# Performance work log

Measured on AMD Instinct MI355X. Metric: run time of the kernel, lower is better.

The kernel has to match this reference:

```python
import jax, jax.numpy as jnp
import numpy as np

NEG_SLOPE = 0.2  # PyG GATConv default leaky_relu slope


def _gat_conv(x, src, dst, W, a_src, a_dst, b, num_nodes, heads, out_dim):
    # x: [N, F_in] -> h: [N, H, C]
    h = (x @ W).reshape(num_nodes, heads, out_dim)
    alpha_src = jnp.sum(h * a_src, axis=-1)  # [N, H]
    alpha_dst = jnp.sum(h * a_dst, axis=-1)  # [N, H]
    # per-edge unnormalized attention logits [E, H]
    alpha = jax.nn.leaky_relu(alpha_src[src] + alpha_dst[dst], NEG_SLOPE)
    # segment softmax over incoming edges of each destination node
    amax = jax.ops.segment_max(alpha, dst, num_segments=num_nodes)  # [N, H]
    e = jnp.exp(alpha - amax[dst])
    denom = jax.ops.segment_sum(e, dst, num_segments=num_nodes)  # [N, H]
    attn = e / denom[dst]  # every node has a self-loop, denom > 0
    # scatter-aggregate messages [E, H, C] -> [N, H, C]
    msg = h[src] * attn[:, :, None]
    out = jax.ops.segment_sum(msg, dst, num_segments=num_nodes)
    return out.reshape(num_nodes, heads * out_dim) + b


def setup_inputs() -> dict:
    key = jax.random.key(0)
    ks = jax.random.split(key, 12)
    N, F_in, H, C1, C2 = 100000, 128, 4, 32, 16
    E = 1600000
    x = jax.random.normal(ks[0], (N, F_in), dtype=jnp.float32)
    edge_index = jax.random.randint(ks[1], (2, E), 0, N, dtype=jnp.int64)
    s1 = 1.0 / np.sqrt(F_in)
    s2 = 1.0 / np.sqrt(H * C1)
    W1 = jax.random.normal(ks[2], (F_in, H * C1), dtype=jnp.float32) * s1
    a_src1 = jax.random.normal(ks[3], (H, C1), dtype=jnp.float32) * s1
    a_dst1 = jax.random.normal(ks[4], (H, C1), dtype=jnp.float32) * s1
    b1 = jnp.zeros((H * C1,), dtype=jnp.float32)
    W2 = jax.random.normal(ks[5], (H * C1, C2), dtype=jnp.float32) * s2
    a_src2 = jax.random.normal(ks[6], (1, C2), dtype=jnp.float32) * s2
    a_dst2 = jax.random.normal(ks[7], (1, C2), dtype=jnp.float32) * s2
    b2 = jnp.zeros((C2,), dtype=jnp.float32)
    return {"x": x, "edge_index": edge_index, "W1": W1, "a_src1": a_src1,
            "a_dst1": a_dst1, "b1": b1, "W2": W2, "a_src2": a_src2,
            "a_dst2": a_dst2, "b2": b2}


def reference(x, edge_index, W1, a_src1, a_dst1, b1, W2, a_src2, a_dst2, b2):
    N = x.shape[0]
    H, C1 = a_src1.shape
    C2 = a_src2.shape[1]
    # PyG GATConv default add_self_loops=True
    loop = jnp.arange(N, dtype=edge_index.dtype)
    src = jnp.concatenate([edge_index[0], loop])
    dst = jnp.concatenate([edge_index[1], loop])
    # dropout_ratio=0.0 / eval mode -> F.dropout is identity
    h = _gat_conv(x, src, dst, W1, a_src1, a_dst1, b1, N, H, C1)
    h = jax.nn.elu(h)
    out = _gat_conv(h, src, dst, W2, a_src2, a_dst2, b2, N, 1, C2)
    return out
```

## Files before the change

kernel.cpp:

```cpp
#include <hip/hip_runtime.h>
#include <cstdint>
#include <cstddef>

#define NEG_SLOPE 0.2f


__device__ __forceinline__ int edge_at(const void* ei, long long idx, int is64) {
    if (is64) return (int)((const long long*)ei)[idx];
    return ((const int*)ei)[idx];
}

__global__ void detect_fmt_kernel(const void* ei, int* flag) {
    if (threadIdx.x == 0 && blockIdx.x == 0) {
        const unsigned* u = (const unsigned*)ei;
        int zc = 0;
        for (int i = 0; i < 128; ++i) zc += (u[2 * i + 1] == 0u);
        *flag = (zc >= 100) ? 1 : 0;
    }
}

__global__ __launch_bounds__(256) void gemm1_kernel(
    const float* __restrict__ x, const float* __restrict__ W,
    const float* __restrict__ a_src, const float* __restrict__ a_dst,
    float* __restrict__ h1, float* __restrict__ asrc, float* __restrict__ adst,
    int N) {
    __shared__ float As[128][33];
    __shared__ float Bs[32][128];
    const int tid = threadIdx.x;
    const int tx = tid & 15, ty = tid >> 4;
    const int base = blockIdx.x * 128;

    float acc[8][8];
#pragma unroll
    for (int i = 0; i < 8; ++i)
#pragma unroll
        for (int j = 0; j < 8; ++j) acc[i][j] = 0.f;

    for (int kb = 0; kb < 128; kb += 32) {
        {
            const int r0 = tid >> 3;
            const int q  = tid & 7;
#pragma unroll
            for (int p = 0; p < 4; ++p) {
                int r = r0 + p * 32;
                int gr = base + r;
                float4 v = make_float4(0.f, 0.f, 0.f, 0.f);
                if (gr < N) v = *(const float4*)(x + (size_t)gr * 128 + kb + q * 4);
                As[r][q * 4 + 0] = v.x; As[r][q * 4 + 1] = v.y;
                As[r][q * 4 + 2] = v.z; As[r][q * 4 + 3] = v.w;
            }
        }
        {
            const int k0 = tid >> 5;
            const int f  = tid & 31;
#pragma unroll
            for (int p = 0; p < 4; ++p) {
                int kk = k0 + p * 8;
                float4 v = *(const float4*)(W + (size_t)(kb + kk) * 128 + f * 4);
                *(float4*)&Bs[kk][f * 4] = v;
            }
        }
        __syncthreads();
#pragma unroll 4
        for (int kk = 0; kk < 32; ++kk) {
            float a[8];
#pragma unroll
            for (int i = 0; i < 8; ++i) a[i] = As[ty * 8 + i][kk];
            float4 b0 = *(const float4*)&Bs[kk][tx * 4];
            float4 b1 = *(const float4*)&Bs[kk][64 + tx * 4];
            float b[8] = {b0.x, b0.y, b0.z, b0.w, b1.x, b1.y, b1.z, b1.w};
#pragma unroll
            for (int i = 0; i < 8; ++i)
#pragma unroll
                for (int j = 0; j < 8; ++j)
                    acc[i][j] = fmaf(a[i], b[j], acc[i][j]);
        }
        __syncthreads();
    }

    float asv[8], adv[8];
#pragma unroll
    for (int jj = 0; jj < 4; ++jj) {
        asv[jj]     = a_src[tx * 4 + jj];
        asv[4 + jj] = a_src[64 + tx * 4 + jj];
        adv[jj]     = a_dst[tx * 4 + jj];
        adv[4 + jj] = a_dst[64 + tx * 4 + jj];
    }

#pragma unroll
    for (int i = 0; i < 8; ++i) {
        int gr = base + ty * 8 + i;
        float p0s = 0.f, p1s = 0.f, p0d = 0.f, p1d = 0.f;
#pragma unroll
        for (int jj = 0; jj < 4; ++jj) {
            p0s = fmaf(acc[i][jj],     asv[jj],     p0s);
            p0d = fmaf(acc[i][jj],     adv[jj],     p0d);
            p1s = fmaf(acc[i][4 + jj], asv[4 + jj], p1s);
            p1d = fmaf(acc[i][4 + jj], adv[4 + jj], p1d);
        }
#pragma unroll
        for (int off = 1; off < 8; off <<= 1) {
            p0s += __shfl_xor(p0s, off);
            p0d += __shfl_xor(p0d, off);
            p1s += __shfl_xor(p1s, off);
            p1d += __shfl_xor(p1d, off);
        }
        if (gr < N) {
            float4 o0 = make_float4(acc[i][0], acc[i][1], acc[i][2], acc[i][3]);
            float4 o1 = make_float4(acc[i][4], acc[i][5], acc[i][6], acc[i][7]);
            *(float4*)(h1 + (size_t)gr * 128 + tx * 4) = o0;
            *(float4*)(h1 + (size_t)gr * 128 + 64 + tx * 4) = o1;
            if ((tx & 7) == 0) {
                int hlo = tx >> 3;
                asrc[gr * 4 + hlo]     = p0s;
                adst[gr * 4 + hlo]     = p0d;
                asrc[gr * 4 + 2 + hlo] = p1s;
                adst[gr * 4 + 2 + hlo] = p1d;
            }
        }
    }
}

__global__ void deg_init_kernel(int* deg, int* cursor, int N) {
    int i = blockIdx.x * 256 + threadIdx.x;
    if (i < N) { deg[i] = 1; cursor[i] = 0; }
}

__global__ void hist_kernel(const void* ei, int* deg, int E, const int* flag) {
    int i = blockIdx.x * 256 + threadIdx.x;
    if (i < E) {
        int is64 = *flag;
        int d = edge_at(ei, (long long)E + i, is64);
        atomicAdd(&deg[d], 1);
    }
}

__global__ void reduce_kernel(const int* __restrict__ deg, int* bsums, int N) {
    __shared__ int s[256];
    int tid = threadIdx.x;
    int base = blockIdx.x * 1024 + tid * 4;
    int t = 0;
#pragma unroll
    for (int u = 0; u < 4; ++u) { int idx = base + u; if (idx < N) t += deg[idx]; }
    s[tid] = t;
    __syncthreads();
    for (int off = 128; off; off >>= 1) {
        if (tid < off) s[tid] += s[tid + off];
        __syncthreads();
    }
    if (tid == 0) bsums[blockIdx.x] = s[0];
}

__global__ void scan_bsums_kernel(int* bsums, int* rowptr, int nb, int N) {
    if (threadIdx.x == 0 && blockIdx.x == 0) {
        int run = 0;
        for (int b = 0; b < nb; ++b) { int t = bsums[b]; bsums[b] = run; run += t; }
        rowptr[N] = run;
    }
}

__global__ void scan_write_kernel(const int* __restrict__ deg,
                                  const int* __restrict__ bsums,
                                  int* __restrict__ rowptr, int N) {
    __shared__ int s[256];
    int tid = threadIdx.x;
    int base_i = blockIdx.x * 1024 + tid * 4;
    int v[4]; int t = 0;
#pragma unroll
    for (int u = 0; u < 4; ++u) {
        int idx = base_i + u;
        v[u] = (idx < N) ? deg[idx] : 0;
        t += v[u];
    }
    s[tid] = t;
    __syncthreads();
    for (int off = 1; off < 256; off <<= 1) {
        int tv = (tid >= off) ? s[tid - off] : 0;
        __syncthreads();
        s[tid] += tv;
        __syncthreads();
    }
    int excl = (tid == 0) ? 0 : s[tid - 1];
    int p = bsums[blockIdx.x] + excl;
#pragma unroll
    for (int u = 0; u < 4; ++u) {
        int idx = base_i + u;
        if (idx < N) rowptr[idx] = p;
        p += v[u];
    }
}

__global__ void scatter_kernel(const void* ei, const int* __restrict__ rowptr,
                               int* cursor, int* __restrict__ srcs,
                               int E, int ET, const int* flag) {
    int i = blockIdx.x * 256 + threadIdx.x;
    if (i < ET) {
        int is64 = *flag;
        int s, d;
        if (i < E) {
            s = edge_at(ei, i, is64);
            d = edge_at(ei, (long long)E + i, is64);
        } else {
            s = d = i - E;
        }
        int pos = rowptr[d] + atomicAdd(&cursor[d], 1);
        srcs[pos] = s;
    }
}

__global__ __launch_bounds__(128) void agg1_kernel(
    const float* __restrict__ h1, const float* __restrict__ asrc,
    const float* __restrict__ adst, const int* __restrict__ rowptr,
    const int* __restrict__ srcs, const float* __restrict__ b1,
    float* __restrict__ g, int N) {
    int d = blockIdx.x;
    int tid = threadIdx.x;
    int h = tid >> 5, l = tid & 31;
    int start = rowptr[d], end = rowptr[d + 1];
    int deg = end - start;
    float ad = adst[d * 4 + h];

    float m = -1e30f;
    for (int j = start + l; j < end; j += 32) {
        float t = asrc[srcs[j] * 4 + h] + ad;
        t = (t > 0.f) ? t : NEG_SLOPE * t;
        m = fmaxf(m, t);
    }
#pragma unroll
    for (int off = 16; off; off >>= 1) m = fmaxf(m, __shfl_xor(m, off, 32));

    float acc = 0.f, lsum = 0.f;
    for (int cb = 0; cb < deg; cb += 32) {
        int cl = min(32, deg - cb);
        float wv = 0.f; int sv = 0;
        if (l < cl) {
            sv = srcs[start + cb + l];
            float t = asrc[sv * 4 + h] + ad;
            t = (t > 0.f) ? t : NEG_SLOPE * t;
            wv = __expf(t - m);
        }
        for (int e = 0; e < cl; ++e) {
            float w = __shfl(wv, e, 32);
            int s = __shfl(sv, e, 32);
            lsum += w;
            acc = fmaf(w, h1[(size_t)s * 128 + tid], acc);
        }
    }
    float r = acc / lsum + b1[tid];
    g[(size_t)d * 128 + tid] = (r > 0.f) ? r : expm1f(r);
}

__global__ __launch_bounds__(256) void gemm2_kernel(
    const float* __restrict__ g, const float* __restrict__ W2,
    const float* __restrict__ a_src2, const float* __restrict__ a_dst2,
    float* __restrict__ h2, float* __restrict__ asrc2, float* __restrict__ adst2,
    int N) {
    __shared__ float W2s[128 * 16];
    __shared__ float gs[16][132];
    int tid = threadIdx.x;
#pragma unroll
    for (int u = 0; u < 8; ++u) W2s[u * 256 + tid] = W2[u * 256 + tid];
    int base = blockIdx.x * 16;
#pragma unroll
    for (int p = 0; p < 2; ++p) {
        int q = tid + p * 256;
        int r = q >> 5, c4 = q & 31;
        int gr = base + r;
        float4 v = make_float4(0.f, 0.f, 0.f, 0.f);
        if (gr < N) v = *(const float4*)(g + (size_t)gr * 128 + c4 * 4);
        *(float4*)&gs[r][c4 * 4] = v;
    }
    __syncthreads();
    int ln = tid >> 4, c = tid & 15;
    int n = base + ln;
    float acc = 0.f;
#pragma unroll 8
    for (int k = 0; k < 128; ++k)
        acc = fmaf(gs[ln][k], W2s[k * 16 + c], acc);
    float s1 = acc * a_src2[c];
    float s2 = acc * a_dst2[c];
#pragma unroll
    for (int off = 8; off; off >>= 1) {
        s1 += __shfl_xor(s1, off, 16);
        s2 += __shfl_xor(s2, off, 16);
    }
    if (n < N) {
        h2[(size_t)n * 16 + c] = acc;
        if (c == 0) { asrc2[n] = s1; adst2[n] = s2; }
    }
}

__global__ __launch_bounds__(64) void agg2_kernel(
    const float* __restrict__ h2, const float* __restrict__ asrc2,
    const float* __restrict__ adst2, const int* __restrict__ rowptr,
    const int* __restrict__ srcs, const float* __restrict__ b2,
    float* __restrict__ out, int N) {
    int tid = threadIdx.x;
    int d = blockIdx.x * 4 + (tid >> 4);
    int c = tid & 15;
    if (d >= N) return;
    int start = rowptr[d], end = rowptr[d + 1];
    int deg = end - start;
    float ad = adst2[d];

    float m = -1e30f;
    for (int j = start + c; j < end; j += 16) {
        float t = asrc2[srcs[j]] + ad;
        t = (t > 0.f) ? t : NEG_SLOPE * t;
        m = fmaxf(m, t);
    }
#pragma unroll
    for (int off = 8; off; off >>= 1) m = fmaxf(m, __shfl_xor(m, off, 16));

    float acc = 0.f, lsum = 0.f;
    for (int cb = 0; cb < deg; cb += 16) {
        int cl = min(16, deg - cb);
        float wv = 0.f; int sv = 0;
        if (c < cl) {
            sv = srcs[start + cb + c];
            float t = asrc2[sv] + ad;
            t = (t > 0.f) ? t : NEG_SLOPE * t;
            wv = __expf(t - m);
        }
        for (int e = 0; e < cl; ++e) {
            float w = __shfl(wv, e, 16);
            int s = __shfl(sv, e, 16);
            lsum += w;
            acc = fmaf(w, h2[(size_t)s * 16 + c], acc);
        }
    }
    out[(size_t)d * 16 + c] = acc / lsum + b2[c];
}

extern "C" void kernel_launch(void* const* d_in, const int* in_sizes, int n_in,
                              void* d_out, int out_size, void* d_ws, size_t ws_size,
                              hipStream_t stream) {
    const float* x      = (const float*)d_in[0];
    const void*  ei     = d_in[1];
    const float* W1     = (const float*)d_in[2];
    const float* a_src1 = (const float*)d_in[3];
    const float* a_dst1 = (const float*)d_in[4];
    const float* b1     = (const float*)d_in[5];
    const float* W2     = (const float*)d_in[6];
    const float* a_src2 = (const float*)d_in[7];
    const float* a_dst2 = (const float*)d_in[8];
    const float* b2     = (const float*)d_in[9];

    const int N  = in_sizes[0] / 128;
    const int E  = in_sizes[1] / 2;
    const int ET = E + N;

    char* w = (char*)d_ws;
    size_t off = 0;
    auto alloc = [&](size_t bytes) -> char* {
        char* p = w + off;
        off = (off + bytes + 255) & ~(size_t)255;
        return p;
    };
    float* h1     = (float*)alloc((size_t)N * 128 * 4);
    float* g      = (float*)alloc((size_t)N * 128 * 4);
    float* asrc1  = (float*)alloc((size_t)N * 4 * 4);
    float* adst1  = (float*)alloc((size_t)N * 4 * 4);
    int*   deg    = (int*)alloc((size_t)N * 4);
    int*   cursor = (int*)alloc((size_t)N * 4);
    int*   rowptr = (int*)alloc((size_t)(N + 1) * 4);
    int*   srcs   = (int*)alloc((size_t)ET * 4);
    int*   bsums  = (int*)alloc(4096);
    int*   flag   = (int*)alloc(256);
    float* h2    = h1;
    float* asrc2 = h1 + (size_t)N * 16;
    float* adst2 = asrc2 + N;

    const int nb = (N + 1023) / 1024;

    detect_fmt_kernel<<<1, 1, 0, stream>>>(ei, flag);
    gemm1_kernel<<<(N + 127) / 128, 256, 0, stream>>>(x, W1, a_src1, a_dst1,
                                                      h1, asrc1, adst1, N);
    deg_init_kernel<<<(N + 255) / 256, 256, 0, stream>>>(deg, cursor, N);
    hist_kernel<<<(E + 255) / 256, 256, 0, stream>>>(ei, deg, E, flag);
    reduce_kernel<<<nb, 256, 0, stream>>>(deg, bsums, N);
    scan_bsums_kernel<<<1, 1, 0, stream>>>(bsums, rowptr, nb, N);
    scan_write_kernel<<<nb, 256, 0, stream>>>(deg, bsums, rowptr, N);
    scatter_kernel<<<(ET + 255) / 256, 256, 0, stream>>>(ei, rowptr, cursor, srcs, E, ET, flag);
    agg1_kernel<<<N, 128, 0, stream>>>(h1, asrc1, adst1, rowptr, srcs, b1, g, N);
    gemm2_kernel<<<(N + 15) / 16, 256, 0, stream>>>(g, W2, a_src2, a_dst2, h2, asrc2, adst2, N);
    agg2_kernel<<<(N + 3) / 4, 64, 0, stream>>>(h2, asrc2, adst2, rowptr, srcs, b2, (float*)d_out, N);
}
```

Before: 620.1 us.

## Unroll aggregation gathers, transpose GEMM1 A tile, parallelize block-sum scan

The aggregation kernels now issue eight independent neighbor gathers per step into separate accumulators, which exposes memory-level parallelism that the single serial FMA chain hid. The softmax denominator is summed once per lane and reduced with shuffles at the end. GEMM1 stores its A tile transposed in shared memory so each thread reads it with float4 loads, and the single-thread block-sum scan becomes a 128-thread parallel scan. agg2 also moves to 256-thread blocks covering 16 nodes each, at the cost of higher register use and a different floating-point summation order.

Measured after the change: 549.8 us. -11.3%, faster.

```diff
diff --git a/kernel.cpp b/kernel.cpp
--- a/kernel.cpp
+++ b/kernel.cpp
@@ -24,7 +24,7 @@
     const float* __restrict__ a_src, const float* __restrict__ a_dst,
     float* __restrict__ h1, float* __restrict__ asrc, float* __restrict__ adst,
     int N) {
-    __shared__ float As[128][33];
+    __shared__ float As2[32][132];
     __shared__ float Bs[32][128];
     const int tid = threadIdx.x;
     const int tx = tid & 15, ty = tid >> 4;
@@ -46,8 +46,8 @@
                 int gr = base + r;
                 float4 v = make_float4(0.f, 0.f, 0.f, 0.f);
                 if (gr < N) v = *(const float4*)(x + (size_t)gr * 128 + kb + q * 4);
-                As[r][q * 4 + 0] = v.x; As[r][q * 4 + 1] = v.y;
-                As[r][q * 4 + 2] = v.z; As[r][q * 4 + 3] = v.w;
+                As2[q * 4 + 0][r] = v.x; As2[q * 4 + 1][r] = v.y;
+                As2[q * 4 + 2][r] = v.z; As2[q * 4 + 3][r] = v.w;
             }
         }
         {
@@ -63,9 +63,9 @@
         __syncthreads();
 #pragma unroll 4
         for (int kk = 0; kk < 32; ++kk) {
-            float a[8];
-#pragma unroll
-            for (int i = 0; i < 8; ++i) a[i] = As[ty * 8 + i][kk];
+            float4 a0 = *(const float4*)&As2[kk][ty * 8];
+            float4 a1 = *(const float4*)&As2[kk][ty * 8 + 4];
+            float a[8] = {a0.x, a0.y, a0.z, a0.w, a1.x, a1.y, a1.z, a1.w};
             float4 b0 = *(const float4*)&Bs[kk][tx * 4];
             float4 b1 = *(const float4*)&Bs[kk][64 + tx * 4];
             float b[8] = {b0.x, b0.y, b0.z, b0.w, b1.x, b1.y, b1.z, b1.w};
@@ -152,11 +152,29 @@
 }
 
 __global__ void scan_bsums_kernel(int* bsums, int* rowptr, int nb, int N) {
-    if (threadIdx.x == 0 && blockIdx.x == 0) {
-        int run = 0;
-        for (int b = 0; b < nb; ++b) { int t = bsums[b]; bsums[b] = run; run += t; }
-        rowptr[N] = run;
-    }
+    __shared__ int s[128];
+    __shared__ int carry;
+    int tid = threadIdx.x;
+    if (tid == 0) carry = 0;
+    __syncthreads();
+    for (int base = 0; base < nb; base += 128) {
+        int idx = base + tid;
+        int v = (idx < nb) ? bsums[idx] : 0;
+        s[tid] = v;
+        __syncthreads();
+        for (int off = 1; off < 128; off <<= 1) {
+            int t = (tid >= off) ? s[tid - off] : 0;
+            __syncthreads();
+            s[tid] += t;
+            __syncthreads();
+        }
+        int excl = carry + ((tid == 0) ? 0 : s[tid - 1]);
+        if (idx < nb) bsums[idx] = excl;
+        __syncthreads();
+        if (tid == 0) carry += s[127];
+        __syncthreads();
+    }
+    if (tid == 0) rowptr[N] = carry;
 }
 
 __global__ void scan_write_kernel(const int* __restrict__ deg,
@@ -229,7 +247,10 @@
 #pragma unroll
     for (int off = 16; off; off >>= 1) m = fmaxf(m, __shfl_xor(m, off, 32));
 
-    float acc = 0.f, lsum = 0.f;
+    float a0 = 0.f, a1 = 0.f, a2 = 0.f, a3 = 0.f;
+    float a4 = 0.f, a5 = 0.f, a6 = 0.f, a7 = 0.f;
+    float lsum = 0.f;
+    const float* h1c = h1 + tid;
     for (int cb = 0; cb < deg; cb += 32) {
         int cl = min(32, deg - cb);
         float wv = 0.f; int sv = 0;
@@ -239,13 +260,35 @@
             t = (t > 0.f) ? t : NEG_SLOPE * t;
             wv = __expf(t - m);
         }
-        for (int e = 0; e < cl; ++e) {
+        lsum += wv;
+        int e = 0;
+        for (; e + 8 <= cl; e += 8) {
+            int  s0 = __shfl(sv, e + 0, 32), s1 = __shfl(sv, e + 1, 32);
+            int  s2 = __shfl(sv, e + 2, 32), s3 = __shfl(sv, e + 3, 32);
+            int  s4 = __shfl(sv, e + 4, 32), s5 = __shfl(sv, e + 5, 32);
+            int  s6 = __shfl(sv, e + 6, 32), s7 = __shfl(sv, e + 7, 32);
+            float w0 = __shfl(wv, e + 0, 32), w1 = __shfl(wv, e + 1, 32);
+            float w2 = __shfl(wv, e + 2, 32), w3 = __shfl(wv, e + 3, 32);
+            float w4 = __shfl(wv, e + 4, 32), w5 = __shfl(wv, e + 5, 32);
+            float w6 = __shfl(wv, e + 6, 32), w7 = __shfl(wv, e + 7, 32);
+            a0 = fmaf(w0, h1c[(size_t)s0 * 128], a0);
+            a1 = fmaf(w1, h1c[(size_t)s1 * 128], a1);
+            a2 = fmaf(w2, h1c[(size_t)s2 * 128], a2);
+            a3 = fmaf(w3, h1c[(size_t)s3 * 128], a3);
+            a4 = fmaf(w4, h1c[(size_t)s4 * 128], a4);
+            a5 = fmaf(w5, h1c[(size_t)s5 * 128], a5);
+            a6 = fmaf(w6, h1c[(size_t)s6 * 128], a6);
+            a7 = fmaf(w7, h1c[(size_t)s7 * 128], a7);
+        }
+        for (; e < cl; ++e) {
+            int s = __shfl(sv, e, 32);
             float w = __shfl(wv, e, 32);
-            int s = __shfl(sv, e, 32);
-            lsum += w;
-            acc = fmaf(w, h1[(size_t)s * 128 + tid], acc);
-        }
-    }
+            a0 = fmaf(w, h1c[(size_t)s * 128], a0);
+        }
+    }
+#pragma unroll
+    for (int off = 16; off; off >>= 1) lsum += __shfl_xor(lsum, off, 32);
+    float acc = ((a0 + a1) + (a2 + a3)) + ((a4 + a5) + (a6 + a7));
     float r = acc / lsum + b1[tid];
     g[(size_t)d * 128 + tid] = (r > 0.f) ? r : expm1f(r);
 }
@@ -290,13 +333,13 @@
     }
 }
 
-__global__ __launch_bounds__(64) void agg2_kernel(
+__global__ __launch_bounds__(256) void agg2_kernel(
     const float* __restrict__ h2, const float* __restrict__ asrc2,
     const float* __restrict__ adst2, const int* __restrict__ rowptr,
     const int* __restrict__ srcs, const float* __restrict__ b2,
     float* __restrict__ out, int N) {
     int tid = threadIdx.x;
-    int d = blockIdx.x * 4 + (tid >> 4);
+    int d = blockIdx.x * 16 + (tid >> 4);
     int c = tid & 15;
     if (d >= N) return;
     int start = rowptr[d], end = rowptr[d + 1];
@@ -312,7 +355,10 @@
 #pragma unroll
     for (int off = 8; off; off >>= 1) m = fmaxf(m, __shfl_xor(m, off, 16));
 
-    float acc = 0.f, lsum = 0.f;
+    float a0 = 0.f, a1 = 0.f, a2 = 0.f, a3 = 0.f;
+    float a4 = 0.f, a5 = 0.f, a6 = 0.f, a7 = 0.f;
+    float lsum = 0.f;
+    const float* h2c = h2 + c;
     for (int cb = 0; cb < deg; cb += 16) {
         int cl = min(16, deg - cb);
         float wv = 0.f; int sv = 0;
@@ -322,13 +368,35 @@
             t = (t > 0.f) ? t : NEG_SLOPE * t;
             wv = __expf(t - m);
         }
-        for (int e = 0; e < cl; ++e) {
+        lsum += wv;
+        int e = 0;
+        for (; e + 8 <= cl; e += 8) {
+            int  s0 = __shfl(sv, e + 0, 16), s1 = __shfl(sv, e + 1, 16);
+            int  s2 = __shfl(sv, e + 2, 16), s3 = __shfl(sv, e + 3, 16);
+            int  s4 = __shfl(sv, e + 4, 16), s5 = __shfl(sv, e + 5, 16);
+            int  s6 = __shfl(sv, e + 6, 16), s7 = __shfl(sv, e + 7, 16);
+            float w0 = __shfl(wv, e + 0, 16), w1 = __shfl(wv, e + 1, 16);
+            float w2 = __shfl(wv, e + 2, 16), w3 = __shfl(wv, e + 3, 16);
+            float w4 = __shfl(wv, e + 4, 16), w5 = __shfl(wv, e + 5, 16);
+            float w6 = __shfl(wv, e + 6, 16), w7 = __shfl(wv, e + 7, 16);
+            a0 = fmaf(w0, h2c[(size_t)s0 * 16], a0);
+            a1 = fmaf(w1, h2c[(size_t)s1 * 16], a1);
+            a2 = fmaf(w2, h2c[(size_t)s2 * 16], a2);
+            a3 = fmaf(w3, h2c[(size_t)s3 * 16], a3);
+            a4 = fmaf(w4, h2c[(size_t)s4 * 16], a4);
+            a5 = fmaf(w5, h2c[(size_t)s5 * 16], a5);
+            a6 = fmaf(w6, h2c[(size_t)s6 * 16], a6);
+            a7 = fmaf(w7, h2c[(size_t)s7 * 16], a7);
+        }
+        for (; e < cl; ++e) {
+            int s = __shfl(sv, e, 16);
             float w = __shfl(wv, e, 16);
-            int s = __shfl(sv, e, 16);
-            lsum += w;
-            acc = fmaf(w, h2[(size_t)s * 16 + c], acc);
-        }
-    }
+            a0 = fmaf(w, h2c[(size_t)s * 16], a0);
+        }
+    }
+#pragma unroll
+    for (int off = 8; off; off >>= 1) lsum += __shfl_xor(lsum, off, 16);
+    float acc = ((a0 + a1) + (a2 + a3)) + ((a4 + a5) + (a6 + a7));
     out[(size_t)d * 16 + c] = acc / lsum + b2[c];
 }
 
@@ -379,10 +447,10 @@
     deg_init_kernel<<<(N + 255) / 256, 256, 0, stream>>>(deg, cursor, N);
     hist_kernel<<<(E + 255) / 256, 256, 0, stream>>>(ei, deg, E, flag);
     reduce_kernel<<<nb, 256, 0, stream>>>(deg, bsums, N);
-    scan_bsums_kernel<<<1, 1, 0, stream>>>(bsums, rowptr, nb, N);
+    scan_bsums_kernel<<<1, 128, 0, stream>>>(bsums, rowptr, nb, N);
     scan_write_kernel<<<nb, 256, 0, stream>>>(deg, bsums, rowptr, N);
     scatter_kernel<<<(ET + 255) / 256, 256, 0, stream>>>(ei, rowptr, cursor, srcs, E, ET, flag);
     agg1_kernel<<<N, 128, 0, stream>>>(h1, asrc1, adst1, rowptr, srcs, b1, g, N);
     gemm2_kernel<<<(N + 15) / 16, 256, 0, stream>>>(g, W2, a_src2, a_dst2, h2, asrc2, adst2, N);
-    agg2_kernel<<<(N + 3) / 4, 64, 0, stream>>>(h2, asrc2, adst2, rowptr, srcs, b2, (float*)d_out, N);
-}
+    agg2_kernel<<<(N + 15) / 16, 256, 0, stream>>>(h2, asrc2, adst2, rowptr, srcs, b2, (float*)d_out, N);
+}
```
